# Optimization experiments

Measured on AMD Instinct MI355X. Metric: run time of the kernel, lower is better.

## Reference

```python
import jax, jax.numpy as jnp
import numpy as np

N_NODES = 50000
N_EDGES = 800000
IN_FEATS = 64
HIDDEN = 64
NUM_CLASSES = 8


def setup_inputs() -> dict:
    key = jax.random.key(0)
    ks = jax.random.split(key, 6)
    embeds = jax.random.normal(ks[0], (N_NODES, IN_FEATS), dtype=jnp.float32)
    edge_index = jax.random.randint(ks[1], (2, N_EDGES), 0, N_NODES, dtype=jnp.int32)
    sc1 = 1.0 / np.sqrt(IN_FEATS)
    sc2 = 1.0 / np.sqrt(HIDDEN)
    W_l1 = jax.random.normal(ks[2], (IN_FEATS, HIDDEN), dtype=jnp.float32) * sc1
    b_l1 = jnp.zeros((HIDDEN,), dtype=jnp.float32)
    W_r1 = jax.random.normal(ks[3], (IN_FEATS, HIDDEN), dtype=jnp.float32) * sc1
    W_l2 = jax.random.normal(ks[4], (HIDDEN, NUM_CLASSES), dtype=jnp.float32) * sc2
    b_l2 = jnp.zeros((NUM_CLASSES,), dtype=jnp.float32)
    W_r2 = jax.random.normal(ks[5], (HIDDEN, NUM_CLASSES), dtype=jnp.float32) * sc2
    return {"embeds": embeds, "edge_index": edge_index,
            "W_l1": W_l1, "b_l1": b_l1, "W_r1": W_r1,
            "W_l2": W_l2, "b_l2": b_l2, "W_r2": W_r2}


def _sage_conv(x, src, dst, W_l, b_l, W_r):
    # PyG SAGEConv('mean'): lin_l(mean_{j->i} x_j) + lin_r(x_i); lin_r has no bias.
    msg = x[src]                                                   # [E, F] gather
    agg = jax.ops.segment_sum(msg, dst, num_segments=N_NODES)      # [N, F]
    deg = jax.ops.segment_sum(jnp.ones((src.shape[0],), x.dtype), dst,
                              num_segments=N_NODES)                # [N]
    agg = agg / jnp.maximum(deg, 1.0)[:, None]
    return agg @ W_l + b_l + x @ W_r


def reference(embeds, edge_index, W_l1, b_l1, W_r1, W_l2, b_l2, W_r2):
    src, dst = edge_index[0], edge_index[1]
    h = _sage_conv(embeds, src, dst, W_l1, b_l1, W_r1)
    # dropout between layers is identity at inference; source applies no ReLU
    h = _sage_conv(h, src, dst, W_l2, b_l2, W_r2)
    return h
```

## Files before the change

kernel.cpp:

```cpp
#include <hip/hip_runtime.h>
#include <hip/hip_bf16.h>
#include <cstddef>

#define N_FEATS 64
#define NBKT_SHIFT 8
#define EPB 4096
#define CAP 6144

typedef __attribute__((ext_vector_type(8))) short bf16x8;
typedef __attribute__((ext_vector_type(4))) float f32x4;

__device__ __forceinline__ unsigned f2bf(float f) {
    unsigned x = __float_as_uint(f);
    return (x + 0x7fffu + ((x >> 16) & 1u)) >> 16;
}

__global__ __launch_bounds__(256) void k_init(
        const float* __restrict__ Wl1, const float* __restrict__ bl1,
        const float* __restrict__ Wr1, const float* __restrict__ Wl2,
        const float* __restrict__ bl2, const float* __restrict__ Wr2,
        unsigned short* __restrict__ Wc, float* __restrict__ bvec,
        int* __restrict__ cursor, int nbkt) {
    int tid = threadIdx.x;
    int k = tid & 63, jg = tid >> 6;
    const float* W1 = (jg < 2) ? Wl1 : Wr1;
    const float* W2 = (jg & 1) ? Wr2 : Wl2;
    float acc[8] = {0.f,0.f,0.f,0.f,0.f,0.f,0.f,0.f};
    for (int m = 0; m < 64; ++m) {
        float w1 = W1[k * 64 + m];
        #pragma unroll
        for (int jj = 0; jj < 8; ++jj) acc[jj] += w1 * W2[m * 8 + jj];
    }
    #pragma unroll
    for (int jj = 0; jj < 8; ++jj)
        Wc[k * 32 + jg * 8 + jj] = (unsigned short)f2bf(acc[jj]);
    if (tid < 16) {
        const float* W2b = (tid < 8) ? Wl2 : Wr2;
        float a = 0.f;
        for (int m = 0; m < 64; ++m) a += bl1[m] * W2b[m * 8 + (tid & 7)];
        if (tid >= 8) a += bl2[tid - 8];
        bvec[tid] = a;
    }
    if (tid < nbkt) cursor[tid] = 0;
}

__global__ __launch_bounds__(256) void k_split_gemm(
        const int* __restrict__ src, const int* __restrict__ dst,
        int* __restrict__ cursor, unsigned* __restrict__ pairs,
        int nEdges, int nbkt, int nb1,
        const float* __restrict__ x,
        const unsigned short* __restrict__ Wc,
        const float* __restrict__ bvec,
        unsigned short* __restrict__ G,
        float* __restrict__ T,
        int nNodes, int nStrips) {
    __shared__ unsigned spr[EPB];
    __shared__ int lh[256];
    __shared__ int lcur[256];
    int tid = threadIdx.x, b = blockIdx.x;

    if (b < nb1) {
        lh[tid] = 0;
        __syncthreads();
        int base = b * EPB;
        int m = nEdges - base; if (m > EPB) m = EPB;
        for (int j = tid; j < m; j += 256) {
            unsigned d = (unsigned)dst[base + j];
            spr[j] = ((unsigned)src[base + j] << 16) | d;
            atomicAdd(&lh[d >> NBKT_SHIFT], 1);
        }
        __syncthreads();
        if (tid < nbkt) lcur[tid] = atomicAdd(&cursor[tid], lh[tid]);
        __syncthreads();
        for (int j = tid; j < m; j += 256) {
            unsigned pr = spr[j];
            unsigned d = pr & 0xffffu;
            int bkt = d >> NBKT_SHIFT;
            int pos = atomicAdd(&lcur[bkt], 1);
            if (pos < CAP)
                pairs[(size_t)bkt * CAP + pos] = ((pr >> 16) << 8) | (d & 255u);
        }
        return;
    }

    int w  = tid >> 6;
    int l  = tid & 63;
    int fc = l & 15;
    int kg = l >> 4;
    bf16x8 bf[2][2];
    #pragma unroll
    for (int ct = 0; ct < 2; ++ct)
        #pragma unroll
        for (int kh = 0; kh < 2; ++kh)
            #pragma unroll
            for (int i = 0; i < 8; ++i) {
                int k = kh * 32 + kg * 8 + i;
                bf[ct][kh][i] = (short)Wc[k * 32 + ct * 16 + fc];
            }
    float bias = bvec[fc];

    for (int strip = b - nb1; strip < nStrips; strip += gridDim.x - nb1) {
        int node0 = strip * 64;
        int arow = node0 + w * 16 + fc;
        int ar = (arow < nNodes) ? arow : (nNodes - 1);
        const float* xp = x + (size_t)ar * 64 + kg * 8;
        float4 xa = *(const float4*)(xp);
        float4 xb = *(const float4*)(xp + 4);
        float4 xc = *(const float4*)(xp + 32);
        float4 xd = *(const float4*)(xp + 36);
        bf16x8 a0, a1;
        a0[0]=(short)f2bf(xa.x); a0[1]=(short)f2bf(xa.y);
        a0[2]=(short)f2bf(xa.z); a0[3]=(short)f2bf(xa.w);
        a0[4]=(short)f2bf(xb.x); a0[5]=(short)f2bf(xb.y);
        a0[6]=(short)f2bf(xb.z); a0[7]=(short)f2bf(xb.w);
        a1[0]=(short)f2bf(xc.x); a1[1]=(short)f2bf(xc.y);
        a1[2]=(short)f2bf(xc.z); a1[3]=(short)f2bf(xc.w);
        a1[4]=(short)f2bf(xd.x); a1[5]=(short)f2bf(xd.y);
        a1[6]=(short)f2bf(xd.z); a1[7]=(short)f2bf(xd.w);

        f32x4 d0 = {0.f, 0.f, 0.f, 0.f};
        f32x4 d1 = {0.f, 0.f, 0.f, 0.f};
        d0 = __builtin_amdgcn_mfma_f32_16x16x32_bf16(a0, bf[0][0], d0, 0, 0, 0);
        d0 = __builtin_amdgcn_mfma_f32_16x16x32_bf16(a1, bf[0][1], d0, 0, 0, 0);
        d1 = __builtin_amdgcn_mfma_f32_16x16x32_bf16(a0, bf[1][0], d1, 0, 0, 0);
        d1 = __builtin_amdgcn_mfma_f32_16x16x32_bf16(a1, bf[1][1], d1, 0, 0, 0);

        #pragma unroll
        for (int r = 0; r < 4; ++r) {
            int node = node0 + w * 16 + kg * 4 + r;
            if (node < nNodes) {
                G[(size_t)node * 16 + fc] = (unsigned short)f2bf(d0[r]);
                T[(size_t)node * 16 + fc] = d1[r] + bias;
            }
        }
    }
}

__global__ __launch_bounds__(256) void k_fsort(
        const unsigned* __restrict__ pairs,
        const int* __restrict__ cursor,
        int* __restrict__ counts,
        int* __restrict__ offsets,
        unsigned short* __restrict__ sorted_src,
        int nNodes, int nbkt) {
    __shared__ int cnt[256];
    __shared__ int scanbuf[256];
    __shared__ int cur[256];
    int tid = threadIdx.x, b = blockIdx.x;
    int bStart = b * CAP;
    int m = cursor[b]; if (m > CAP) m = CAP;
    cnt[tid] = 0;
    __syncthreads();
    for (int e = tid; e < m; e += 256) {
        atomicAdd(&cnt[pairs[bStart + e] & 255u], 1);
    }
    __syncthreads();
    int v = cnt[tid];
    scanbuf[tid] = v;
    __syncthreads();
    for (int d = 1; d < 256; d <<= 1) {
        int t = (tid >= d) ? scanbuf[tid - d] : 0;
        __syncthreads();
        scanbuf[tid] += t;
        __syncthreads();
    }
    int excl = scanbuf[tid] - v;
    int node = (b << NBKT_SHIFT) + tid;
    if (node < nNodes) { counts[node] = v; offsets[node] = bStart + excl; }
    cur[tid] = bStart + excl;
    __syncthreads();
    for (int e = tid; e < m; e += 256) {
        unsigned pr = pairs[bStart + e];
        int pos = atomicAdd(&cur[pr & 255u], 1);
        sorted_src[pos] = (unsigned short)(pr >> 8);
    }
}

__global__ __launch_bounds__(256) void k_gather2(
        const unsigned* __restrict__ G,
        const float* __restrict__ T,
        const int* __restrict__ counts,
        const int* __restrict__ offsets,
        const unsigned short* __restrict__ ss,
        unsigned* __restrict__ pbf,
        float* __restrict__ q,
        int nNodes) {
    int tid  = threadIdx.x;
    int wave = tid >> 6, lane = tid & 63;
    int half = lane >> 5;
    int eg   = (lane >> 2) & 7;
    int t4   = lane & 3;
    int node = blockIdx.x * 8 + wave * 2 + half;
    if (node >= nNodes) return;
    int cnt = counts[node], off = offsets[node];
    const uint2* G2 = (const uint2*)G;

    float a0 = 0.f, a1 = 0.f, a2 = 0.f, a3 = 0.f;
    int id = (eg < cnt) ? (int)ss[off + eg] : -1;
    for (int base = 0; base < cnt; base += 8) {
        int en = base + 8 + eg;
        int idn = (en < cnt) ? (int)ss[off + en] : -1;
        if (id >= 0) {
            uint2 r = G2[(size_t)id * 4 + t4];
            a0 += __uint_as_float(r.x << 16);
            a1 += __uint_as_float(r.x & 0xffff0000u);
            a2 += __uint_as_float(r.y << 16);
            a3 += __uint_as_float(r.y & 0xffff0000u);
        }
        id = idn;
    }
    a0 += __shfl_xor(a0, 4);  a1 += __shfl_xor(a1, 4);
    a2 += __shfl_xor(a2, 4);  a3 += __shfl_xor(a3, 4);
    a0 += __shfl_xor(a0, 8);  a1 += __shfl_xor(a1, 8);
    a2 += __shfl_xor(a2, 8);  a3 += __shfl_xor(a3, 8);
    a0 += __shfl_xor(a0, 16); a1 += __shfl_xor(a1, 16);
    a2 += __shfl_xor(a2, 16); a3 += __shfl_xor(a3, 16);

    if (eg == 0) {
        float inv = 1.0f / fmaxf((float)cnt, 1.0f);
        float4 tv = *(const float4*)&T[(size_t)node * 16 + t4 * 4];
        float r0 = a0 * inv + tv.x;
        float r1 = a1 * inv + tv.y;
        float r2 = a2 * inv + tv.z;
        float r3 = a3 * inv + tv.w;
        if (t4 < 2) {
            uint2 o;
            o.x = f2bf(r0) | (f2bf(r1) << 16);
            o.y = f2bf(r2) | (f2bf(r3) << 16);
            *(uint2*)(pbf + (size_t)node * 4 + t4 * 2) = o;
        } else {
            float4 o; o.x = r0; o.y = r1; o.z = r2; o.w = r3;
            *(float4*)(q + (size_t)node * 8 + (t4 - 2) * 4) = o;
        }
    }
}

__global__ __launch_bounds__(256) void k_final(
        const unsigned* __restrict__ pbf,
        const float* __restrict__ q,
        const int* __restrict__ counts,
        const int* __restrict__ offsets,
        const unsigned short* __restrict__ ss,
        float* __restrict__ out,
        int nNodes) {
    int tid  = threadIdx.x;
    int wave = tid >> 6, lane = tid & 63;
    int half = lane >> 5;
    int eg   = (lane >> 1) & 15;
    int t2   = lane & 1;
    int node = blockIdx.x * 8 + wave * 2 + half;
    if (node >= nNodes) return;
    int cnt = counts[node], off = offsets[node];
    const uint2* P2 = (const uint2*)pbf;

    float a0 = 0.f, a1 = 0.f, a2 = 0.f, a3 = 0.f;
    int id = (eg < cnt) ? (int)ss[off + eg] : -1;
    for (int base = 0; base < cnt; base += 16) {
        int en = base + 16 + eg;
        int idn = (en < cnt) ? (int)ss[off + en] : -1;
        if (id >= 0) {
            uint2 r = P2[(size_t)id * 2 + t2];
            a0 += __uint_as_float(r.x << 16);
            a1 += __uint_as_float(r.x & 0xffff0000u);
            a2 += __uint_as_float(r.y << 16);
            a3 += __uint_as_float(r.y & 0xffff0000u);
        }
        id = idn;
    }
    a0 += __shfl_xor(a0, 2);  a1 += __shfl_xor(a1, 2);
    a2 += __shfl_xor(a2, 2);  a3 += __shfl_xor(a3, 2);
    a0 += __shfl_xor(a0, 4);  a1 += __shfl_xor(a1, 4);
    a2 += __shfl_xor(a2, 4);  a3 += __shfl_xor(a3, 4);
    a0 += __shfl_xor(a0, 8);  a1 += __shfl_xor(a1, 8);
    a2 += __shfl_xor(a2, 8);  a3 += __shfl_xor(a3, 8);
    a0 += __shfl_xor(a0, 16); a1 += __shfl_xor(a1, 16);
    a2 += __shfl_xor(a2, 16); a3 += __shfl_xor(a3, 16);

    if (eg == 0) {
        float inv = 1.0f / fmaxf((float)cnt, 1.0f);
        float4 qv = *(const float4*)&q[(size_t)node * 8 + t2 * 4];
        float4 o;
        o.x = a0 * inv + qv.x; o.y = a1 * inv + qv.y;
        o.z = a2 * inv + qv.z; o.w = a3 * inv + qv.w;
        *(float4*)(out + (size_t)node * 8 + t2 * 4) = o;
    }
}

static inline size_t align256(size_t v) { return (v + 255) & ~(size_t)255; }

extern "C" void kernel_launch(void* const* d_in, const int* in_sizes, int n_in,
                              void* d_out, int out_size, void* d_ws, size_t ws_size,
                              hipStream_t stream) {
    const float* embeds = (const float*)d_in[0];
    const int*   ei     = (const int*)d_in[1];
    const float* Wl1    = (const float*)d_in[2];
    const float* bl1    = (const float*)d_in[3];
    const float* Wr1    = (const float*)d_in[4];
    const float* Wl2    = (const float*)d_in[5];
    const float* bl2    = (const float*)d_in[6];
    const float* Wr2    = (const float*)d_in[7];

    const int N = in_sizes[0] / N_FEATS;
    const int E = in_sizes[1] / 2;
    const int* src = ei;
    const int* dst = ei + E;

    const int NBKT = (N + 255) >> NBKT_SHIFT;
    const int NB1  = (E + EPB - 1) / EPB;
    const int NSTRIPS = (N + 63) / 64;

    char* ws = (char*)d_ws;
    size_t off = 0;
    int*            cursor     = (int*)(ws + off); off += align256((size_t)NBKT * sizeof(int));
    int*            counts     = (int*)(ws + off); off += align256((size_t)N * sizeof(int));
    int*            offsets    = (int*)(ws + off); off += align256((size_t)N * sizeof(int));
    unsigned short* Wc         = (unsigned short*)(ws + off); off += align256(64 * 32 * sizeof(unsigned short));
    float*          bvec       = (float*)(ws + off); off += align256(16 * sizeof(float));
    unsigned*       pairs      = (unsigned*)(ws + off); off += align256((size_t)NBKT * CAP * sizeof(unsigned));
    unsigned short* sorted_src = (unsigned short*)(ws + off); off += align256((size_t)NBKT * CAP * sizeof(unsigned short));
    unsigned*       G          = (unsigned*)(ws + off); off += align256((size_t)N * 16 * sizeof(unsigned short));
    float*          T          = (float*)(ws + off); off += align256((size_t)N * 16 * sizeof(float));
    unsigned*       pbf        = (unsigned*)(ws + off); off += align256((size_t)N * 4 * sizeof(unsigned));
    float*          q          = (float*)(ws + off); off += align256((size_t)N * 8 * sizeof(float));
    (void)ws_size;

    k_init<<<1, 256, 0, stream>>>(Wl1, bl1, Wr1, Wl2, bl2, Wr2, Wc, bvec,
                                  cursor, NBKT);
    k_split_gemm<<<NB1 + NSTRIPS, 256, 0, stream>>>(
        src, dst, cursor, pairs, E, NBKT, NB1,
        embeds, Wc, bvec, (unsigned short*)G, T, N, NSTRIPS);
    k_fsort<<<NBKT, 256, 0, stream>>>(pairs, cursor, counts, offsets,
                                      sorted_src, N, NBKT);
    k_gather2<<<(N + 7) / 8, 256, 0, stream>>>(G, T, counts, offsets, sorted_src,
                                               pbf, q, N);
    k_final<<<(N + 7) / 8, 256, 0, stream>>>(pbf, q, counts, offsets, sorted_src,
                                             (float*)d_out, N);
}
```

Baseline: 62.74 us.

## Fuse bucket sort with first-layer gather using shared-memory sorted sources

Merges the per-bucket counting sort and the layer-1 neighbor gather into one kernel with 1024-thread blocks. Sorted source ids are kept in LDS so the gather reads them from shared memory instead of global memory, and one kernel launch disappears. In exchange, parallelism drops to about 196 blocks of 1024 threads, each handling 256 nodes serially in 8 iterations. The larger LDS footprint may also limit occupancy and load balance.

```diff
diff --git a/kernel.cpp b/kernel.cpp
--- a/kernel.cpp
+++ b/kernel.cpp
@@ -136,101 +136,108 @@
     }
 }
 
-__global__ __launch_bounds__(256) void k_fsort(
+__global__ __launch_bounds__(1024) void k_fsort_gather2(
         const unsigned* __restrict__ pairs,
         const int* __restrict__ cursor,
+        const unsigned* __restrict__ G,
+        const float* __restrict__ T,
         int* __restrict__ counts,
         int* __restrict__ offsets,
         unsigned short* __restrict__ sorted_src,
+        unsigned* __restrict__ pbf,
+        float* __restrict__ q,
         int nNodes, int nbkt) {
-    __shared__ int cnt[256];
+    __shared__ unsigned short ss[CAP];
+    __shared__ int cntA[256];
     __shared__ int scanbuf[256];
+    __shared__ int loff[256];
     __shared__ int cur[256];
     int tid = threadIdx.x, b = blockIdx.x;
     int bStart = b * CAP;
     int m = cursor[b]; if (m > CAP) m = CAP;
-    cnt[tid] = 0;
-    __syncthreads();
-    for (int e = tid; e < m; e += 256) {
-        atomicAdd(&cnt[pairs[bStart + e] & 255u], 1);
-    }
-    __syncthreads();
-    int v = cnt[tid];
-    scanbuf[tid] = v;
+
+    if (tid < 256) cntA[tid] = 0;
+    __syncthreads();
+    for (int e = tid; e < m; e += 1024)
+        atomicAdd(&cntA[pairs[bStart + e] & 255u], 1);
+    __syncthreads();
+    int v = 0;
+    if (tid < 256) { v = cntA[tid]; scanbuf[tid] = v; }
     __syncthreads();
     for (int d = 1; d < 256; d <<= 1) {
-        int t = (tid >= d) ? scanbuf[tid - d] : 0;
-        __syncthreads();
-        scanbuf[tid] += t;
-        __syncthreads();
-    }
-    int excl = scanbuf[tid] - v;
-    int node = (b << NBKT_SHIFT) + tid;
-    if (node < nNodes) { counts[node] = v; offsets[node] = bStart + excl; }
-    cur[tid] = bStart + excl;
-    __syncthreads();
-    for (int e = tid; e < m; e += 256) {
+        int t = (tid < 256 && tid >= d) ? scanbuf[tid - d] : 0;
+        __syncthreads();
+        if (tid < 256) scanbuf[tid] += t;
+        __syncthreads();
+    }
+    if (tid < 256) {
+        int excl = scanbuf[tid] - v;
+        loff[tid] = excl;
+        cur[tid] = excl;
+        int node = (b << NBKT_SHIFT) + tid;
+        if (node < nNodes) { counts[node] = v; offsets[node] = bStart + excl; }
+    }
+    __syncthreads();
+    for (int e = tid; e < m; e += 1024) {
         unsigned pr = pairs[bStart + e];
         int pos = atomicAdd(&cur[pr & 255u], 1);
-        sorted_src[pos] = (unsigned short)(pr >> 8);
-    }
-}
-
-__global__ __launch_bounds__(256) void k_gather2(
-        const unsigned* __restrict__ G,
-        const float* __restrict__ T,
-        const int* __restrict__ counts,
-        const int* __restrict__ offsets,
-        const unsigned short* __restrict__ ss,
-        unsigned* __restrict__ pbf,
-        float* __restrict__ q,
-        int nNodes) {
-    int tid  = threadIdx.x;
+        unsigned short sv = (unsigned short)(pr >> 8);
+        ss[pos] = sv;
+        sorted_src[bStart + pos] = sv;
+    }
+    __syncthreads();
+
     int wave = tid >> 6, lane = tid & 63;
     int half = lane >> 5;
     int eg   = (lane >> 2) & 7;
     int t4   = lane & 3;
-    int node = blockIdx.x * 8 + wave * 2 + half;
-    if (node >= nNodes) return;
-    int cnt = counts[node], off = offsets[node];
     const uint2* G2 = (const uint2*)G;
 
-    float a0 = 0.f, a1 = 0.f, a2 = 0.f, a3 = 0.f;
-    int id = (eg < cnt) ? (int)ss[off + eg] : -1;
-    for (int base = 0; base < cnt; base += 8) {
-        int en = base + 8 + eg;
-        int idn = (en < cnt) ? (int)ss[off + en] : -1;
-        if (id >= 0) {
-            uint2 r = G2[(size_t)id * 4 + t4];
-            a0 += __uint_as_float(r.x << 16);
-            a1 += __uint_as_float(r.x & 0xffff0000u);
-            a2 += __uint_as_float(r.y << 16);
-            a3 += __uint_as_float(r.y & 0xffff0000u);
-        }
-        id = idn;
-    }
-    a0 += __shfl_xor(a0, 4);  a1 += __shfl_xor(a1, 4);
-    a2 += __shfl_xor(a2, 4);  a3 += __shfl_xor(a3, 4);
-    a0 += __shfl_xor(a0, 8);  a1 += __shfl_xor(a1, 8);
-    a2 += __shfl_xor(a2, 8);  a3 += __shfl_xor(a3, 8);
-    a0 += __shfl_xor(a0, 16); a1 += __shfl_xor(a1, 16);
-    a2 += __shfl_xor(a2, 16); a3 += __shfl_xor(a3, 16);
-
-    if (eg == 0) {
-        float inv = 1.0f / fmaxf((float)cnt, 1.0f);
-        float4 tv = *(const float4*)&T[(size_t)node * 16 + t4 * 4];
-        float r0 = a0 * inv + tv.x;
-        float r1 = a1 * inv + tv.y;
-        float r2 = a2 * inv + tv.z;
-        float r3 = a3 * inv + tv.w;
-        if (t4 < 2) {
-            uint2 o;
-            o.x = f2bf(r0) | (f2bf(r1) << 16);
-            o.y = f2bf(r2) | (f2bf(r3) << 16);
-            *(uint2*)(pbf + (size_t)node * 4 + t4 * 2) = o;
-        } else {
-            float4 o; o.x = r0; o.y = r1; o.z = r2; o.w = r3;
-            *(float4*)(q + (size_t)node * 8 + (t4 - 2) * 4) = o;
+    #pragma unroll 1
+    for (int it = 0; it < 8; ++it) {
+        int nl = it * 32 + wave * 2 + half;
+        int node = (b << NBKT_SHIFT) + nl;
+        if (node >= nNodes) continue;
+        int cnt_n = cntA[nl];
+        int lo = loff[nl];
+
+        float a0 = 0.f, a1 = 0.f, a2 = 0.f, a3 = 0.f;
+        int id = (eg < cnt_n) ? (int)ss[lo + eg] : -1;
+        for (int base = 0; base < cnt_n; base += 8) {
+            int en = base + 8 + eg;
+            int idn = (en < cnt_n) ? (int)ss[lo + en] : -1;
+            if (id >= 0) {
+                uint2 r = G2[(size_t)id * 4 + t4];
+                a0 += __uint_as_float(r.x << 16);
+                a1 += __uint_as_float(r.x & 0xffff0000u);
+                a2 += __uint_as_float(r.y << 16);
+                a3 += __uint_as_float(r.y & 0xffff0000u);
+            }
+            id = idn;
+        }
+        a0 += __shfl_xor(a0, 4);  a1 += __shfl_xor(a1, 4);
+        a2 += __shfl_xor(a2, 4);  a3 += __shfl_xor(a3, 4);
+        a0 += __shfl_xor(a0, 8);  a1 += __shfl_xor(a1, 8);
+        a2 += __shfl_xor(a2, 8);  a3 += __shfl_xor(a3, 8);
+        a0 += __shfl_xor(a0, 16); a1 += __shfl_xor(a1, 16);
+        a2 += __shfl_xor(a2, 16); a3 += __shfl_xor(a3, 16);
+
+        if (eg == 0) {
+            float inv = 1.0f / fmaxf((float)cnt_n, 1.0f);
+            float4 tv = *(const float4*)&T[(size_t)node * 16 + t4 * 4];
+            float r0 = a0 * inv + tv.x;
+            float r1 = a1 * inv + tv.y;
+            float r2 = a2 * inv + tv.z;
+            float r3 = a3 * inv + tv.w;
+            if (t4 < 2) {
+                uint2 o;
+                o.x = f2bf(r0) | (f2bf(r1) << 16);
+                o.y = f2bf(r2) | (f2bf(r3) << 16);
+                *(uint2*)(pbf + (size_t)node * 4 + t4 * 2) = o;
+            } else {
+                float4 o; o.x = r0; o.y = r1; o.z = r2; o.w = r3;
+                *(float4*)(q + (size_t)node * 8 + (t4 - 2) * 4) = o;
+            }
         }
     }
 }
@@ -329,10 +336,8 @@
     k_split_gemm<<<NB1 + NSTRIPS, 256, 0, stream>>>(
         src, dst, cursor, pairs, E, NBKT, NB1,
         embeds, Wc, bvec, (unsigned short*)G, T, N, NSTRIPS);
-    k_fsort<<<NBKT, 256, 0, stream>>>(pairs, cursor, counts, offsets,
-                                      sorted_src, N, NBKT);
-    k_gather2<<<(N + 7) / 8, 256, 0, stream>>>(G, T, counts, offsets, sorted_src,
-                                               pbf, q, N);
+    k_fsort_gather2<<<NBKT, 1024, 0, stream>>>(
+        pairs, cursor, G, T, counts, offsets, sorted_src, pbf, q, N, NBKT);
     k_final<<<(N + 7) / 8, 256, 0, stream>>>(pbf, q, counts, offsets, sorted_src,
                                              (float*)d_out, N);
 }
```

New measurement: 62.91 us. No clear change (+0.3%).
